# Performance work log

Measured on AMD Instinct MI355X. Metric: run time of the kernel, lower is better.

## Reference

```python
import jax, jax.numpy as jnp
import numpy as np

B, N, D = 8, 4096, 1024
S, K = 4, 16            # n_slices, per-slice codebook size (2^(16/4))
d = D // S              # slice_dim = 256
BETA = 0.25


def setup_inputs() -> dict:
    key = jax.random.key(0)
    k1, k2 = jax.random.split(key)
    h = jax.random.normal(k1, (B, N, D), dtype=jnp.float32)
    # nn.init.uniform_(codebook.weight, -1/K, 1/K)
    codebooks = jax.random.uniform(k2, (S, K, d), dtype=jnp.float32,
                                   minval=-1.0 / K, maxval=1.0 / K)
    return {"h": h, "codebooks": codebooks}


def reference(h, codebooks):
    Bb, Nn, Dd = h.shape
    Ss, Kk, dd = codebooks.shape
    sg = jax.lax.stop_gradient

    # sliced DVQ: view h as [B,N,S,d]
    ze = h.reshape(Bb, Nn, Ss, dd)

    # pairwise squared distances per slice: [B,N,S,K]
    dist = ((ze ** 2).sum(-1, keepdims=True)
            + (codebooks ** 2).sum(-1)[None, None, :, :]
            - 2.0 * jnp.einsum('bnsd,skd->bnsk', ze, codebooks))
    ids = jnp.argmin(dist, axis=-1)                         # [B,N,S] int

    # gather nearest codes: [B,N,S,d]
    zq = codebooks[jnp.arange(Ss)[None, None, :], ids]

    # per-slice VQ losses (mse over that slice), summed over slices
    loss_cb = jnp.mean((zq - sg(ze)) ** 2, axis=(0, 1, 3))  # [S]
    loss_cm = jnp.mean((ze - sg(zq)) ** 2, axis=(0, 1, 3))  # [S]
    vq_total = (loss_cb + BETA * loss_cm).sum()

    # straight-through estimator, concat slices back to [B,N,D]
    z = (ze + sg(zq - ze)).reshape(Bb, Nn, Dd)

    # pack ids: offsets are [1, K, K^2, K^3] since all slice sizes equal
    offsets = (Kk ** jnp.arange(Ss)).astype(jnp.int32)
    ids_packed = (ids.astype(jnp.int32) * offsets).sum(-1)  # [B,N]

    return (z, ids_packed, vq_total)
```

## Files before the change

kernel.cpp:

```cpp
#include <hip/hip_runtime.h>


#define D_FULL 1024
#define SEG 4
#define DSEG 256
#define KC 16
#define TPB_TOKENS 64

__global__ __launch_bounds__(256) void dvq_prep(const float* __restrict__ cb,
                                                double* __restrict__ cbd,
                                                double* __restrict__ c2d,
                                                float* __restrict__ loss_out) {
    int i = threadIdx.x;
    for (int j = i; j < SEG * KC * DSEG; j += 256)
        cbd[j] = (double)cb[j];
    if (i < SEG * KC) {
        const float* p = cb + i * DSEG;
        double s = 0.0;
        for (int j = 0; j < DSEG; ++j) {
            double v = (double)p[j];
            s = fma(v, v, s);
        }
        c2d[i] = s;
    }
    if (i == 0) *loss_out = 0.0f;
}

__global__ __launch_bounds__(256) void dvq_main(const float* __restrict__ h,
                                                const float* __restrict__ cb,
                                                const double* __restrict__ cbd,
                                                const double* __restrict__ c2d,
                                                float* __restrict__ z_out,
                                                float* __restrict__ ids_out,
                                                float* __restrict__ loss_out) {
    __shared__ int ids_lds[TPB_TOKENS][SEG];
    __shared__ double red[4];

    const int i = threadIdx.x;
    const int lane = i & 63;
    const int w = i >> 6;
    const int s = __builtin_amdgcn_readfirstlane(w);

    const long tok_base = (long)blockIdx.x * TPB_TOKENS;
    const long tok = tok_base + lane;

    const float4* zp = (const float4*)(h + tok * D_FULL + (long)s * DSEG);
    const double* cbs = cbd + s * (KC * DSEG);

    double dot[KC];
#pragma unroll
    for (int k = 0; k < KC; ++k) dot[k] = 0.0;
    double ze2 = 0.0;

    for (int c = 0; c < DSEG / 4; ++c) {
        float4 z4 = zp[c];
        double z0 = (double)z4.x, z1 = (double)z4.y;
        double z2 = (double)z4.z, z3 = (double)z4.w;
        ze2 = fma(z0, z0, ze2);
        ze2 = fma(z1, z1, ze2);
        ze2 = fma(z2, z2, ze2);
        ze2 = fma(z3, z3, ze2);
#pragma unroll
        for (int k = 0; k < KC; ++k) {
            const double* ck = cbs + k * DSEG + c * 4;
            double a = dot[k];
            a = fma(z0, ck[0], a);
            a = fma(z1, ck[1], a);
            a = fma(z2, ck[2], a);
            a = fma(z3, ck[3], a);
            dot[k] = a;
        }
    }

    const double* c2s = c2d + s * KC;
    double best = c2s[0] - 2.0 * dot[0];
    int bk = 0;
#pragma unroll
    for (int k = 1; k < KC; ++k) {
        double sc = c2s[k] - 2.0 * dot[k];
        if (sc < best) { best = sc; bk = k; }
    }
    ids_lds[lane][w] = bk;

    double mind = ze2 + best;
#pragma unroll
    for (int off = 32; off > 0; off >>= 1)
        mind += __shfl_down(mind, off, 64);
    if (lane == 0) red[w] = mind;

    __syncthreads();

    if (i == 0) {
        double tot = red[0] + red[1] + red[2] + red[3];
        atomicAdd(loss_out, (float)(tot * (1.25 / 8388608.0)));
    }

    for (int r = 0; r < TPB_TOKENS; ++r) {
        int k = ids_lds[r][w];
        float4 v = ((const float4*)(cb + (s * KC + k) * DSEG))[lane];
        ((float4*)(z_out + (tok_base + r) * D_FULL))[i] = v;
    }

    if (i < TPB_TOKENS) {
        int p = ids_lds[i][0] + 16 * ids_lds[i][1] + 256 * ids_lds[i][2] +
                4096 * ids_lds[i][3];
        ids_out[tok_base + i] = (float)p;
    }
}

extern "C" void kernel_launch(void* const* d_in, const int* in_sizes, int n_in,
                              void* d_out, int out_size, void* d_ws, size_t ws_size,
                              hipStream_t stream) {
    const float* h  = (const float*)d_in[0];
    const float* cb = (const float*)d_in[1];

    const int n_h = in_sizes[0];
    const int tokens = n_h / D_FULL;

    float* z_out    = (float*)d_out;
    float* ids_out  = z_out + (size_t)n_h;
    float* loss_out = ids_out + tokens;

    double* cbd = (double*)d_ws;
    double* c2d = cbd + SEG * KC * DSEG;

    dvq_prep<<<1, 256, 0, stream>>>(cb, cbd, c2d, loss_out);
    dvq_main<<<tokens / TPB_TOKENS, 256, 0, stream>>>(h, cb, cbd, c2d, z_out,
                                                      ids_out, loss_out);
}
```

Measured before the change: 295.2 us.

## Split slice dimension across waves and parallelize codebook prep kernel

```diff
diff --git a/kernel.cpp b/kernel.cpp
--- a/kernel.cpp
+++ b/kernel.cpp
@@ -5,25 +5,32 @@
 #define SEG 4
 #define DSEG 256
 #define KC 16
-#define TPB_TOKENS 64
 
 __global__ __launch_bounds__(256) void dvq_prep(const float* __restrict__ cb,
                                                 double* __restrict__ cbd,
                                                 double* __restrict__ c2d,
+                                                float* __restrict__ ids_out,
                                                 float* __restrict__ loss_out) {
-    int i = threadIdx.x;
-    for (int j = i; j < SEG * KC * DSEG; j += 256)
-        cbd[j] = (double)cb[j];
-    if (i < SEG * KC) {
-        const float* p = cb + i * DSEG;
-        double s = 0.0;
-        for (int j = 0; j < DSEG; ++j) {
-            double v = (double)p[j];
-            s = fma(v, v, s);
-        }
-        c2d[i] = s;
-    }
-    if (i == 0) *loss_out = 0.0f;
+    __shared__ double ws[4];
+    const int b = blockIdx.x;
+    const int t = threadIdx.x;
+    const int lane = t & 63;
+    const int w = t >> 6;
+
+    cbd[b * 256 + t] = (double)cb[b * 256 + t];
+
+    ids_out[b * 512 + t] = 0.0f;
+    ids_out[b * 512 + 256 + t] = 0.0f;
+    if (b == 0 && t == 0) *loss_out = 0.0f;
+
+    double v = (double)cb[b * 256 + t];
+    double sq = v * v;
+#pragma unroll
+    for (int off = 32; off > 0; off >>= 1)
+        sq += __shfl_down(sq, off, 64);
+    if (lane == 0) ws[w] = sq;
+    __syncthreads();
+    if (t == 0) c2d[b] = ws[0] + ws[1] + ws[2] + ws[3];
 }
 
 __global__ __launch_bounds__(256) void dvq_main(const float* __restrict__ h,
@@ -33,27 +40,29 @@
                                                 float* __restrict__ z_out,
                                                 float* __restrict__ ids_out,
                                                 float* __restrict__ loss_out) {
-    __shared__ int ids_lds[TPB_TOKENS][SEG];
-    __shared__ double red[4];
+    __shared__ double part[3][64][KC + 1];
+    __shared__ int ids_lds[64];
 
     const int i = threadIdx.x;
     const int lane = i & 63;
     const int w = i >> 6;
-    const int s = __builtin_amdgcn_readfirstlane(w);
+    const int ch = __builtin_amdgcn_readfirstlane(w);
 
-    const long tok_base = (long)blockIdx.x * TPB_TOKENS;
+    const int s = blockIdx.x & 3;
+    const long tok_base = (long)(blockIdx.x >> 2) * 64;
     const long tok = tok_base + lane;
 
-    const float4* zp = (const float4*)(h + tok * D_FULL + (long)s * DSEG);
-    const double* cbs = cbd + s * (KC * DSEG);
+    const float4* zp = (const float4*)(h + tok * D_FULL + (long)s * DSEG + ch * 64);
+    const double* cbs = cbd + s * (KC * DSEG) + ch * 64;
 
     double dot[KC];
 #pragma unroll
     for (int k = 0; k < KC; ++k) dot[k] = 0.0;
     double ze2 = 0.0;
 
-    for (int c = 0; c < DSEG / 4; ++c) {
-        float4 z4 = zp[c];
+#pragma unroll 4
+    for (int j = 0; j < 16; ++j) {
+        float4 z4 = zp[j];
         double z0 = (double)z4.x, z1 = (double)z4.y;
         double z2 = (double)z4.z, z3 = (double)z4.w;
         ze2 = fma(z0, z0, ze2);
@@ -62,7 +71,7 @@
         ze2 = fma(z3, z3, ze2);
 #pragma unroll
         for (int k = 0; k < KC; ++k) {
-            const double* ck = cbs + k * DSEG + c * 4;
+            const double* ck = cbs + k * DSEG + j * 4;
             double a = dot[k];
             a = fma(z0, ck[0], a);
             a = fma(z1, ck[1], a);
@@ -72,39 +81,51 @@
         }
     }
 
-    const double* c2s = c2d + s * KC;
-    double best = c2s[0] - 2.0 * dot[0];
-    int bk = 0;
+    if (w != 0) {
+        double* p = &part[w - 1][lane][0];
 #pragma unroll
-    for (int k = 1; k < KC; ++k) {
-        double sc = c2s[k] - 2.0 * dot[k];
-        if (sc < best) { best = sc; bk = k; }
+        for (int k = 0; k < KC; ++k) p[k] = dot[k];
+        p[KC] = ze2;
     }
-    ids_lds[lane][w] = bk;
-
-    double mind = ze2 + best;
-#pragma unroll
-    for (int off = 32; off > 0; off >>= 1)
-        mind += __shfl_down(mind, off, 64);
-    if (lane == 0) red[w] = mind;
-
     __syncthreads();
 
-    if (i == 0) {
-        double tot = red[0] + red[1] + red[2] + red[3];
-        atomicAdd(loss_out, (float)(tot * (1.25 / 8388608.0)));
+    if (w == 0) {
+#pragma unroll
+        for (int c = 0; c < 3; ++c) {
+            const double* p = &part[c][lane][0];
+#pragma unroll
+            for (int k = 0; k < KC; ++k) dot[k] += p[k];
+            ze2 += p[KC];
+        }
+
+        const double* c2s = c2d + s * KC;
+        double best = c2s[0] - 2.0 * dot[0];
+        int bk = 0;
+#pragma unroll
+        for (int k = 1; k < KC; ++k) {
+            double sc = c2s[k] - 2.0 * dot[k];
+            if (sc < best) { best = sc; bk = k; }
+        }
+        ids_lds[lane] = bk;
+
+        atomicAdd(&ids_out[tok], (float)(bk << (4 * s)));
+
+        double mind = ze2 + best;
+#pragma unroll
+        for (int off = 32; off > 0; off >>= 1)
+            mind += __shfl_down(mind, off, 64);
+        if (lane == 0)
+            atomicAdd(loss_out, (float)(mind * (1.25 / 8388608.0)));
     }
+    __syncthreads();
 
-    for (int r = 0; r < TPB_TOKENS; ++r) {
-        int k = ids_lds[r][w];
-        float4 v = ((const float4*)(cb + (s * KC + k) * DSEG))[lane];
-        ((float4*)(z_out + (tok_base + r) * D_FULL))[i] = v;
-    }
-
-    if (i < TPB_TOKENS) {
-        int p = ids_lds[i][0] + 16 * ids_lds[i][1] + 256 * ids_lds[i][2] +
-                4096 * ids_lds[i][3];
-        ids_out[tok_base + i] = (float)p;
+    const float4* cbf4 = (const float4*)cb;
+#pragma unroll 4
+    for (int r0 = 0; r0 < 16; ++r0) {
+        int r = ch * 16 + r0;
+        int k = ids_lds[r];
+        float4 v = cbf4[(s * KC + k) * (DSEG / 4) + lane];
+        ((float4*)(z_out + (tok_base + r) * D_FULL + (long)s * DSEG))[lane] = v;
     }
 }
 
@@ -124,7 +145,7 @@
     double* cbd = (double*)d_ws;
     double* c2d = cbd + SEG * KC * DSEG;
 
-    dvq_prep<<<1, 256, 0, stream>>>(cb, cbd, c2d, loss_out);
-    dvq_main<<<tokens / TPB_TOKENS, 256, 0, stream>>>(h, cb, cbd, c2d, z_out,
+    dvq_prep<<<64, 256, 0, stream>>>(cb, cbd, c2d, ids_out, loss_out);
+    dvq_main<<<(tokens / 64) * SEG, 256, 0, stream>>>(h, cb, cbd, c2d, z_out,
                                                       ids_out, loss_out);
 }
```

Result: faster. 264.6 us (-10.4%).
